# Optimization experiments

Measured on AMD Instinct MI355X. Metric: run time of the kernel, lower is better.

Reference implementation:

```python
import jax, jax.numpy as jnp
import numpy as np

N = 100000      # nodes
E = 1600000     # edges
D_IN = 128      # input feature dim
H = 128         # hidden dim
C = 2           # num classes
EPS = 1e-5


def setup_inputs() -> dict:
    key = jax.random.key(0)
    ks = jax.random.split(key, 16)
    def lin(k, fan_in, shape):
        return jax.random.uniform(k, shape, jnp.float32, -1.0, 1.0) / np.sqrt(fan_in)
    return {
        "x": jax.random.normal(ks[0], (N, D_IN), jnp.float32),
        "edge_index": jax.random.randint(ks[1], (2, E), 0, N, dtype=jnp.int32),
        # GCNConv weights (lin(x) then normalized aggregation)
        "W1": lin(ks[2], D_IN, (D_IN, H)), "b1": jnp.zeros((H,), jnp.float32),
        "W2": lin(ks[3], H, (H, H)),       "b2": jnp.zeros((H,), jnp.float32),
        "W3": lin(ks[4], H, (H, H)),       "b3": jnp.zeros((H,), jnp.float32),
        # LayerNorms after layers 0 and 1
        "ln1_g": jnp.ones((H,), jnp.float32), "ln1_b": jnp.zeros((H,), jnp.float32),
        "ln2_g": jnp.ones((H,), jnp.float32), "ln2_b": jnp.zeros((H,), jnp.float32),
        # post_mp MLP head (dropout is identity at inference)
        "mp_W1": lin(ks[5], H, (H, H)), "mp_b1": lin(ks[6], H, (H,)),
        "mp_W2": lin(ks[7], H, (H, C)), "mp_b2": lin(ks[8], H, (C,)),
    }


def _layer_norm(x, g, b):
    mu = jnp.mean(x, axis=-1, keepdims=True)
    var = jnp.mean(jnp.square(x - mu), axis=-1, keepdims=True)
    return (x - mu) * jax.lax.rsqrt(var + EPS) * g + b


def reference(x, edge_index, W1, b1, W2, b2, W3, b3,
              ln1_g, ln1_b, ln2_g, ln2_b, mp_W1, mp_b1, mp_W2, mp_b2):
    # --- GCN normalization (computed once; same graph for all layers) ---
    loops = jnp.arange(N, dtype=edge_index.dtype)
    src = jnp.concatenate([edge_index[0], loops])   # A + I, source nodes
    dst = jnp.concatenate([edge_index[1], loops])   # A + I, target nodes
    deg = jax.ops.segment_sum(jnp.ones_like(dst, dtype=x.dtype), dst, num_segments=N)
    dinv = jnp.where(deg > 0, jax.lax.rsqrt(deg), 0.0)
    norm = dinv[src] * dinv[dst]                    # [E+N]

    def gcn(h, W, b):
        h = h @ W                                   # [N, H]
        msg = h[src] * norm[:, None]                # gather + scale: [E+N, H]
        return jax.ops.segment_sum(msg, dst, num_segments=N) + b

    # layer 0
    h = gcn(x, W1, b1)
    h = jax.nn.relu(h)                              # dropout: identity (eval)
    h = _layer_norm(h, ln1_g, ln1_b)
    # layer 1
    h = gcn(h, W2, b2)
    h = jax.nn.relu(h)
    h = _layer_norm(h, ln2_g, ln2_b)
    # layer 2
    h = gcn(h, W3, b3)
    emb = h
    h = jax.nn.relu(h)

    # post_mp: Linear -> Dropout(identity at eval) -> Linear
    out = (h @ mp_W1 + mp_b1) @ mp_W2 + mp_b2
    return emb, jax.nn.log_softmax(out, axis=1)
```

## Files before the change

kernel.cpp:

```cpp
#include <hip/hip_runtime.h>
#include <math.h>

#define HDIM 128
#define EPSLN 1e-5f
#define BSH 8
#define CHUNK 8192
#define EPB 32
#define CAPB 8192

__device__ __forceinline__ unsigned short f2bf(float f) {
  unsigned int u = __float_as_uint(f);
  u = u + 0x7fffu + ((u >> 16) & 1u);
  return (unsigned short)(u >> 16);
}
__device__ __forceinline__ float bf_lo(unsigned int packed) {
  return __uint_as_float(packed << 16);
}
__device__ __forceinline__ float bf_hi(unsigned int packed) {
  return __uint_as_float(packed & 0xffff0000u);
}


__global__ __launch_bounds__(256) void histA_k(const int* __restrict__ dst,
                                               int* __restrict__ bsize, int E_) {
  __shared__ int h[512];
  int t = threadIdx.x;
  h[t] = 0; h[t + 256] = 0;
  __syncthreads();
  int base = blockIdx.x * CHUNK;
  for (int i = 0; i < EPB; i++) {
    int idx = base + i * 256 + t;
    if (idx < E_) atomicAdd(&h[dst[idx] >> BSH], 1);
  }
  __syncthreads();
  int v = h[t];       if (v) atomicAdd(&bsize[t], v);
  v = h[t + 256];     if (v) atomicAdd(&bsize[t + 256], v);
}

__global__ __launch_bounds__(256) void scanA_k(const int* __restrict__ bsize,
                                               int* __restrict__ bbase,
                                               int* __restrict__ bcur,
                                               int* __restrict__ rowptr,
                                               int NB, int n, int E_) {
  __shared__ int sm[512];
  int t = threadIdx.x;
  sm[t] = (t < NB) ? bsize[t] : 0;
  sm[t + 256] = (t + 256 < NB) ? bsize[t + 256] : 0;
  __syncthreads();
  for (int off = 1; off < 512; off <<= 1) {
    int v0 = (t >= off) ? sm[t - off] : 0;
    int v1 = (t + 256 >= off) ? sm[t + 256 - off] : 0;
    __syncthreads();
    sm[t] += v0;
    sm[t + 256] += v1;
    __syncthreads();
  }
  if (t < NB) { int ex = (t == 0) ? 0 : sm[t - 1]; bbase[t] = ex; bcur[t] = ex; }
  int u = t + 256;
  if (u < NB) { int ex = sm[u - 1]; bbase[u] = ex; bcur[u] = ex; }
  if (t == 0) { bbase[NB] = sm[NB - 1]; rowptr[n] = E_; }
}

__global__ __launch_bounds__(256) void scatA_k(const int* __restrict__ src,
                                               const int* __restrict__ dst,
                                               int* __restrict__ bcur,
                                               uint2* __restrict__ binned, int E_) {
  __shared__ int h[512];
  __shared__ int cur[512];
  int t = threadIdx.x;
  h[t] = 0; h[t + 256] = 0;
  __syncthreads();
  int base = blockIdx.x * CHUNK;
  for (int i = 0; i < EPB; i++) {
    int idx = base + i * 256 + t;
    if (idx < E_) atomicAdd(&h[dst[idx] >> BSH], 1);
  }
  __syncthreads();
  int v = h[t];       cur[t] = v ? atomicAdd(&bcur[t], v) : 0;
  v = h[t + 256];     cur[t + 256] = v ? atomicAdd(&bcur[t + 256], v) : 0;
  __syncthreads();
  for (int i = 0; i < EPB; i++) {
    int idx = base + i * 256 + t;
    if (idx < E_) {
      int d = dst[idx];
      int slot = atomicAdd(&cur[d >> BSH], 1);
      binned[slot] = make_uint2((unsigned)src[idx], (unsigned)d);
    }
  }
}

__global__ __launch_bounds__(256) void passB_k(const uint2* __restrict__ binned,
                                               const int* __restrict__ bbase,
                                               int* __restrict__ rowptr,
                                               float* __restrict__ dinv,
                                               int* __restrict__ colx, int n) {
  __shared__ int cnt[256];
  __shared__ int cur[256];
  __shared__ int stage[CAPB];
  int b = blockIdx.x;
  int t = threadIdx.x;
  int beg = bbase[b], end = bbase[b + 1];
  int sz = end - beg;
  int nb0 = b << BSH;
  cnt[t] = 0;
  __syncthreads();
  for (int i = t; i < sz; i += 256) {
    uint2 e = binned[beg + i];
    atomicAdd(&cnt[e.y & 255], 1);
  }
  __syncthreads();
  int myc = cnt[t];
  cur[t] = myc;
  __syncthreads();
  for (int off = 1; off < 256; off <<= 1) {
    int v = (t >= off) ? cur[t - off] : 0;
    __syncthreads();
    cur[t] += v;
    __syncthreads();
  }
  int excl = cur[t] - myc;
  int node = nb0 + t;
  if (node < n) {
    rowptr[node] = beg + excl;
    dinv[node] = rsqrtf((float)(myc + 1));
  }
  __syncthreads();
  cur[t] = excl;
  __syncthreads();
  if (sz <= CAPB) {
    for (int i = t; i < sz; i += 256) {
      uint2 e = binned[beg + i];
      int slot = atomicAdd(&cur[e.y & 255], 1);
      stage[slot] = (int)e.x;
    }
    __syncthreads();
    for (int i = t; i < sz; i += 256) colx[beg + i] = stage[i];
  } else {
    for (int i = t; i < sz; i += 256) {
      uint2 e = binned[beg + i];
      int slot = atomicAdd(&cur[e.y & 255], 1);
      colx[beg + slot] = (int)e.x;
    }
  }
}

__global__ __launch_bounds__(256) void gemm_k(const float* __restrict__ A,
                                              const float* __restrict__ W,
                                              const float* __restrict__ dinv,
                                              unsigned short* __restrict__ Out, int n) {
  __shared__ float hs[64 * HDIM];
  int t = threadIdx.x;
  int rowbase = blockIdx.x * 64;
  const float4* A4 = (const float4*)(A + (size_t)rowbase * HDIM);
  for (int i = 0; i < 8; i++) {
    int fi = t + i * 256;
    int row = rowbase + (fi >> 5);
    float4 v = make_float4(0.f, 0.f, 0.f, 0.f);
    if (row < n) v = A4[fi];
    ((float4*)hs)[fi] = v;
  }
  __syncthreads();

  int tc = t & 31;
  int tr = t >> 5;
  float acc[8][4];
  for (int i = 0; i < 8; i++)
    for (int j = 0; j < 4; j++) acc[i][j] = 0.f;

  const float4* W4 = (const float4*)W;
  for (int k = 0; k < HDIM; k += 4) {
    float4 w0 = W4[(k + 0) * 32 + tc];
    float4 w1 = W4[(k + 1) * 32 + tc];
    float4 w2 = W4[(k + 2) * 32 + tc];
    float4 w3 = W4[(k + 3) * 32 + tc];
    for (int i = 0; i < 8; i++) {
      float4 h4 = *((const float4*)&hs[(tr * 8 + i) * HDIM + k]);
      acc[i][0] += h4.x * w0.x + h4.y * w1.x + h4.z * w2.x + h4.w * w3.x;
      acc[i][1] += h4.x * w0.y + h4.y * w1.y + h4.z * w2.y + h4.w * w3.y;
      acc[i][2] += h4.x * w0.z + h4.y * w1.z + h4.z * w2.z + h4.w * w3.z;
      acc[i][3] += h4.x * w0.w + h4.y * w1.w + h4.z * w2.w + h4.w * w3.w;
    }
  }
  for (int i = 0; i < 8; i++) {
    int row = rowbase + tr * 8 + i;
    if (row < n) {
      float dv = dinv[row];
      ushort4 o;
      o.x = f2bf(acc[i][0] * dv);
      o.y = f2bf(acc[i][1] * dv);
      o.z = f2bf(acc[i][2] * dv);
      o.w = f2bf(acc[i][3] * dv);
      ((ushort4*)(Out + (size_t)row * HDIM))[tc] = o;
    }
  }
}

template <int MODE>
__global__ __launch_bounds__(256) void agg_k(const unsigned short* __restrict__ T,
                                             const int* __restrict__ rowptr,
                                             const int* __restrict__ colx,
                                             const float* __restrict__ dinv,
                                             const float* __restrict__ bias,
                                             const float* __restrict__ lng,
                                             const float* __restrict__ lnb,
                                             float* __restrict__ Out, int n) {
  int wid = (blockIdx.x * 256 + threadIdx.x) >> 6;
  int lane = threadIdx.x & 63;
  if (wid >= n) return;
  int i = wid;
  float di = dinv[i];
  const unsigned int* T32 = (const unsigned int*)T;
  unsigned int us = T32[(size_t)i * 64 + lane];
  float a0x = bf_lo(us), a0y = bf_hi(us);
  float a1x = 0.f, a1y = 0.f;
  int beg = rowptr[i], end = rowptr[i + 1];
  int e = beg;
  int c0 = 0, c1 = 0;
  if (e < end) c0 = colx[e];
  if (e + 1 < end) c1 = colx[e + 1];
  for (; e + 1 < end; e += 2) {
    unsigned int u0 = T32[(size_t)c0 * 64 + lane];
    unsigned int u1 = T32[(size_t)c1 * 64 + lane];
    if (e + 2 < end) c0 = colx[e + 2];
    if (e + 3 < end) c1 = colx[e + 3];
    a0x += bf_lo(u0); a0y += bf_hi(u0);
    a1x += bf_lo(u1); a1y += bf_hi(u1);
  }
  if (e < end) {
    unsigned int u0 = T32[(size_t)c0 * 64 + lane];
    a0x += bf_lo(u0); a0y += bf_hi(u0);
  }
  float2 bb = ((const float2*)bias)[lane];
  float2 acc;
  acc.x = (a0x + a1x) * di + bb.x;
  acc.y = (a0y + a1y) * di + bb.y;
  if (MODE == 0) {
    acc.x = fmaxf(acc.x, 0.f);
    acc.y = fmaxf(acc.y, 0.f);
    float s1 = acc.x + acc.y;
    float s2 = acc.x * acc.x + acc.y * acc.y;
    for (int off = 1; off < 64; off <<= 1) {
      s1 += __shfl_xor(s1, off);
      s2 += __shfl_xor(s2, off);
    }
    float mu = s1 * (1.f / 128.f);
    float var = s2 * (1.f / 128.f) - mu * mu;
    float r = rsqrtf(var + EPSLN);
    float2 gg = ((const float2*)lng)[lane];
    float2 b2 = ((const float2*)lnb)[lane];
    acc.x = (acc.x - mu) * r * gg.x + b2.x;
    acc.y = (acc.y - mu) * r * gg.y + b2.y;
  }
  ((float2*)(Out + (size_t)i * HDIM))[lane] = acc;
}

__global__ __launch_bounds__(256) void head_k(const float* __restrict__ emb,
                                              const float* __restrict__ W1_,
                                              const float* __restrict__ b1_,
                                              const float* __restrict__ W2_,
                                              const float* __restrict__ b2_,
                                              float* __restrict__ outp, int n) {
  __shared__ float hs[64 * HDIM];
  int t = threadIdx.x;
  int rowbase = blockIdx.x * 64;
  const float4* A4 = (const float4*)(emb + (size_t)rowbase * HDIM);
  for (int i = 0; i < 8; i++) {
    int fi = t + i * 256;
    int row = rowbase + (fi >> 5);
    float4 v = make_float4(0.f, 0.f, 0.f, 0.f);
    if (row < n) v = A4[fi];
    v.x = fmaxf(v.x, 0.f);
    v.y = fmaxf(v.y, 0.f);
    v.z = fmaxf(v.z, 0.f);
    v.w = fmaxf(v.w, 0.f);
    ((float4*)hs)[fi] = v;
  }
  __syncthreads();

  int tc = t & 31;
  int tr = t >> 5;
  float acc[8][4];
  float4 binit = ((const float4*)b1_)[tc];
  for (int i = 0; i < 8; i++) {
    acc[i][0] = binit.x; acc[i][1] = binit.y; acc[i][2] = binit.z; acc[i][3] = binit.w;
  }

  const float4* W4 = (const float4*)W1_;
  for (int k = 0; k < HDIM; k += 4) {
    float4 w0 = W4[(k + 0) * 32 + tc];
    float4 w1 = W4[(k + 1) * 32 + tc];
    float4 w2 = W4[(k + 2) * 32 + tc];
    float4 w3 = W4[(k + 3) * 32 + tc];
    for (int i = 0; i < 8; i++) {
      float4 h4 = *((const float4*)&hs[(tr * 8 + i) * HDIM + k]);
      acc[i][0] += h4.x * w0.x + h4.y * w1.x + h4.z * w2.x + h4.w * w3.x;
      acc[i][1] += h4.x * w0.y + h4.y * w1.y + h4.z * w2.y + h4.w * w3.y;
      acc[i][2] += h4.x * w0.z + h4.y * w1.z + h4.z * w2.z + h4.w * w3.z;
      acc[i][3] += h4.x * w0.w + h4.y * w1.w + h4.z * w2.w + h4.w * w3.w;
    }
  }

  float2 w2c[4];
  for (int j = 0; j < 4; j++) w2c[j] = ((const float2*)W2_)[4 * tc + j];
  float o0[8], o1[8];
  for (int i = 0; i < 8; i++) {
    o0[i] = acc[i][0] * w2c[0].x + acc[i][1] * w2c[1].x + acc[i][2] * w2c[2].x + acc[i][3] * w2c[3].x;
    o1[i] = acc[i][0] * w2c[0].y + acc[i][1] * w2c[1].y + acc[i][2] * w2c[2].y + acc[i][3] * w2c[3].y;
  }
  for (int off = 1; off < 32; off <<= 1) {
    for (int i = 0; i < 8; i++) {
      o0[i] += __shfl_xor(o0[i], off);
      o1[i] += __shfl_xor(o1[i], off);
    }
  }
  if (tc == 0) {
    float B0 = b2_[0], B1 = b2_[1];
    for (int i = 0; i < 8; i++) {
      int row = rowbase + tr * 8 + i;
      if (row < n) {
        float a = o0[i] + B0, b = o1[i] + B1;
        float m = fmaxf(a, b);
        float lse = m + logf(expf(a - m) + expf(b - m));
        outp[(size_t)row * 2 + 0] = a - lse;
        outp[(size_t)row * 2 + 1] = b - lse;
      }
    }
  }
}


extern "C" void kernel_launch(void* const* d_in, const int* in_sizes, int n_in,
                              void* d_out, int out_size, void* d_ws, size_t ws_size,
                              hipStream_t stream) {
  const float* x = (const float*)d_in[0];
  const int* ei = (const int*)d_in[1];
  const float* W1 = (const float*)d_in[2];
  const float* b1 = (const float*)d_in[3];
  const float* W2 = (const float*)d_in[4];
  const float* b2 = (const float*)d_in[5];
  const float* W3 = (const float*)d_in[6];
  const float* b3 = (const float*)d_in[7];
  const float* ln1g = (const float*)d_in[8];
  const float* ln1b = (const float*)d_in[9];
  const float* ln2g = (const float*)d_in[10];
  const float* ln2b = (const float*)d_in[11];
  const float* mpW1 = (const float*)d_in[12];
  const float* mpb1 = (const float*)d_in[13];
  const float* mpW2 = (const float*)d_in[14];
  const float* mpb2 = (const float*)d_in[15];

  const int N = in_sizes[0] / HDIM;
  const int E = in_sizes[1] / 2;
  const int* srcp = ei;
  const int* dstp = ei + E;
  const int NB = (N + 255) >> BSH;

  char* p = (char*)d_ws;
  auto carve = [&](size_t bytes) {
    void* r = (void*)p;
    p += (bytes + 255) & ~(size_t)255;
    return r;
  };
  int* bsize = (int*)carve(512 * 4);
  int* bbase = (int*)carve(513 * 4);
  int* bcur = (int*)carve(512 * 4);
  int* rowptr = (int*)carve((size_t)(N + 1) * 4);
  float* dinv = (float*)carve((size_t)N * 4);
  int* colx = (int*)carve((size_t)E * 4);
  uint2* binned = (uint2*)carve((size_t)E * 8);
  unsigned short* bufT = (unsigned short*)carve((size_t)N * HDIM * 2);
  float* bufAct = (float*)carve((size_t)N * HDIM * 4);

  float* emb = (float*)d_out;
  float* logits = (float*)d_out + (size_t)N * HDIM;

  const int chunkG = (E + CHUNK - 1) / CHUNK;

  hipMemsetAsync(bsize, 0, 512 * 4, stream);
  histA_k<<<chunkG, 256, 0, stream>>>(dstp, bsize, E);
  scanA_k<<<1, 256, 0, stream>>>(bsize, bbase, bcur, rowptr, NB, N, E);
  scatA_k<<<chunkG, 256, 0, stream>>>(srcp, dstp, bcur, binned, E);
  passB_k<<<NB, 256, 0, stream>>>(binned, bbase, rowptr, dinv, colx, N);

  const int gemmG = (N + 63) / 64;
  const int aggG = (N * 64 + 255) / 256;

  gemm_k<<<gemmG, 256, 0, stream>>>(x, W1, dinv, bufT, N);
  agg_k<0><<<aggG, 256, 0, stream>>>(bufT, rowptr, colx, dinv, b1, ln1g, ln1b, bufAct, N);
  gemm_k<<<gemmG, 256, 0, stream>>>(bufAct, W2, dinv, bufT, N);
  agg_k<0><<<aggG, 256, 0, stream>>>(bufT, rowptr, colx, dinv, b2, ln2g, ln2b, bufAct, N);
  gemm_k<<<gemmG, 256, 0, stream>>>(bufAct, W3, dinv, bufT, N);
  agg_k<1><<<aggG, 256, 0, stream>>>(bufT, rowptr, colx, dinv, b3, nullptr, nullptr, emb, N);
  head_k<<<gemmG, 256, 0, stream>>>(emb, mpW1, mpb1, mpW2, mpb2, logits, N);
}
```

Baseline: 689.0 us.

## Rewrite feature-transform GEMM with bf16 MFMA and 128-row tiles

The per-layer N×128×128 GEMM is moved from FP32 scalar FMAs to bf16 MFMA 16x16x32 instructions. Activations and weights are converted to bf16 into padded LDS tiles (transposed for W), and each block now covers 128 rows. Each wave handles 32 rows across all 128 output columns. Inputs are rounded to bf16 before the multiply, which lowers precision, and the output is written as scattered 2-byte stores. Each block also re-converts the whole weight matrix.

```diff
diff --git a/kernel.cpp b/kernel.cpp
--- a/kernel.cpp
+++ b/kernel.cpp
@@ -7,6 +7,10 @@
 #define CHUNK 8192
 #define EPB 32
 #define CAPB 8192
+#define LDA 136
+
+typedef __attribute__((ext_vector_type(8))) short bf16x8;
+typedef __attribute__((ext_vector_type(4))) float f32x4;
 
 __device__ __forceinline__ unsigned short f2bf(float f) {
   unsigned int u = __float_as_uint(f);
@@ -148,49 +152,81 @@
                                               const float* __restrict__ W,
                                               const float* __restrict__ dinv,
                                               unsigned short* __restrict__ Out, int n) {
-  __shared__ float hs[64 * HDIM];
-  int t = threadIdx.x;
-  int rowbase = blockIdx.x * 64;
-  const float4* A4 = (const float4*)(A + (size_t)rowbase * HDIM);
-  for (int i = 0; i < 8; i++) {
-    int fi = t + i * 256;
-    int row = rowbase + (fi >> 5);
+  __shared__ short As[128 * LDA];
+  __shared__ short Ws[128 * LDA];
+  int t = threadIdx.x;
+  int rowbase = blockIdx.x * 128;
+
+  #pragma unroll
+  for (int i = 0; i < 64; i++) {
+    int idx = t + i * 256;
+    int k = idx >> 7, c = idx & 127;
+    Ws[c * LDA + k] = (short)f2bf(W[idx]);
+  }
+  const float4* A4 = (const float4*)A;
+  #pragma unroll
+  for (int i = 0; i < 16; i++) {
+    int idx = t + i * 256;
+    int r = idx >> 5, c4 = (idx & 31) << 2;
+    int grow = rowbase + r;
     float4 v = make_float4(0.f, 0.f, 0.f, 0.f);
-    if (row < n) v = A4[fi];
-    ((float4*)hs)[fi] = v;
-  }
-  __syncthreads();
-
-  int tc = t & 31;
-  int tr = t >> 5;
-  float acc[8][4];
-  for (int i = 0; i < 8; i++)
-    for (int j = 0; j < 4; j++) acc[i][j] = 0.f;
-
-  const float4* W4 = (const float4*)W;
-  for (int k = 0; k < HDIM; k += 4) {
-    float4 w0 = W4[(k + 0) * 32 + tc];
-    float4 w1 = W4[(k + 1) * 32 + tc];
-    float4 w2 = W4[(k + 2) * 32 + tc];
-    float4 w3 = W4[(k + 3) * 32 + tc];
-    for (int i = 0; i < 8; i++) {
-      float4 h4 = *((const float4*)&hs[(tr * 8 + i) * HDIM + k]);
-      acc[i][0] += h4.x * w0.x + h4.y * w1.x + h4.z * w2.x + h4.w * w3.x;
-      acc[i][1] += h4.x * w0.y + h4.y * w1.y + h4.z * w2.y + h4.w * w3.y;
-      acc[i][2] += h4.x * w0.z + h4.y * w1.z + h4.z * w2.z + h4.w * w3.z;
-      acc[i][3] += h4.x * w0.w + h4.y * w1.w + h4.z * w2.w + h4.w * w3.w;
-    }
-  }
-  for (int i = 0; i < 8; i++) {
-    int row = rowbase + tr * 8 + i;
-    if (row < n) {
-      float dv = dinv[row];
-      ushort4 o;
-      o.x = f2bf(acc[i][0] * dv);
-      o.y = f2bf(acc[i][1] * dv);
-      o.z = f2bf(acc[i][2] * dv);
-      o.w = f2bf(acc[i][3] * dv);
-      ((ushort4*)(Out + (size_t)row * HDIM))[tc] = o;
+    if (grow < n) v = A4[(size_t)grow * 32 + (idx & 31)];
+    short4 s;
+    s.x = (short)f2bf(v.x); s.y = (short)f2bf(v.y);
+    s.z = (short)f2bf(v.z); s.w = (short)f2bf(v.w);
+    *(short4*)&As[r * LDA + c4] = s;
+  }
+  __syncthreads();
+
+  int wv = t >> 6;
+  int lane = t & 63;
+  int lrow = lane & 15;
+  int lk = (lane >> 4) << 3;
+  int wr0 = wv * 32;
+
+  const short* base0 = &As[(wr0 + lrow) * LDA + lk];
+  const short* base1 = &As[(wr0 + 16 + lrow) * LDA + lk];
+  bf16x8 a00 = *(const bf16x8*)(base0 + 0);
+  bf16x8 a01 = *(const bf16x8*)(base0 + 32);
+  bf16x8 a02 = *(const bf16x8*)(base0 + 64);
+  bf16x8 a03 = *(const bf16x8*)(base0 + 96);
+  bf16x8 a10 = *(const bf16x8*)(base1 + 0);
+  bf16x8 a11 = *(const bf16x8*)(base1 + 32);
+  bf16x8 a12 = *(const bf16x8*)(base1 + 64);
+  bf16x8 a13 = *(const bf16x8*)(base1 + 96);
+
+  int r0 = rowbase + wr0 + ((lane >> 4) << 2);
+  float dv0[4], dv1[4];
+  #pragma unroll
+  for (int r = 0; r < 4; r++) {
+    int g0 = r0 + r, g1 = r0 + 16 + r;
+    dv0[r] = (g0 < n) ? dinv[g0] : 0.f;
+    dv1[r] = (g1 < n) ? dinv[g1] : 0.f;
+  }
+
+  #pragma unroll
+  for (int nt = 0; nt < 8; nt++) {
+    const short* bb = &Ws[(nt * 16 + lrow) * LDA + lk];
+    f32x4 acc0 = {0.f, 0.f, 0.f, 0.f};
+    f32x4 acc1 = {0.f, 0.f, 0.f, 0.f};
+    bf16x8 b0 = *(const bf16x8*)(bb + 0);
+    acc0 = __builtin_amdgcn_mfma_f32_16x16x32_bf16(a00, b0, acc0, 0, 0, 0);
+    acc1 = __builtin_amdgcn_mfma_f32_16x16x32_bf16(a10, b0, acc1, 0, 0, 0);
+    bf16x8 b1 = *(const bf16x8*)(bb + 32);
+    acc0 = __builtin_amdgcn_mfma_f32_16x16x32_bf16(a01, b1, acc0, 0, 0, 0);
+    acc1 = __builtin_amdgcn_mfma_f32_16x16x32_bf16(a11, b1, acc1, 0, 0, 0);
+    bf16x8 b2 = *(const bf16x8*)(bb + 64);
+    acc0 = __builtin_amdgcn_mfma_f32_16x16x32_bf16(a02, b2, acc0, 0, 0, 0);
+    acc1 = __builtin_amdgcn_mfma_f32_16x16x32_bf16(a12, b2, acc1, 0, 0, 0);
+    bf16x8 b3 = *(const bf16x8*)(bb + 96);
+    acc0 = __builtin_amdgcn_mfma_f32_16x16x32_bf16(a03, b3, acc0, 0, 0, 0);
+    acc1 = __builtin_amdgcn_mfma_f32_16x16x32_bf16(a13, b3, acc1, 0, 0, 0);
+    #pragma unroll
+    for (int r = 0; r < 4; r++) {
+      int g0 = r0 + r;
+      if (g0 < n) Out[(size_t)g0 * HDIM + nt * 16 + lrow] = f2bf(acc0[r] * dv0[r]);
+      int g1 = r0 + 16 + r;
+      if (g1 < n) Out[(size_t)g1 * HDIM + nt * 16 + lrow] = f2bf(acc1[r] * dv1[r]);
     }
   }
 }
@@ -382,7 +418,8 @@
   scatA_k<<<chunkG, 256, 0, stream>>>(srcp, dstp, bcur, binned, E);
   passB_k<<<NB, 256, 0, stream>>>(binned, bbase, rowptr, dinv, colx, N);
 
-  const int gemmG = (N + 63) / 64;
+  const int gemmG = (N + 127) / 128;
+  const int headG = (N + 63) / 64;
   const int aggG = (N * 64 + 255) / 256;
 
   gemm_k<<<gemmG, 256, 0, stream>>>(x, W1, dinv, bufT, N);
@@ -391,5 +428,5 @@
   agg_k<0><<<aggG, 256, 0, stream>>>(bufT, rowptr, colx, dinv, b2, ln2g, ln2b, bufAct, N);
   gemm_k<<<gemmG, 256, 0, stream>>>(bufAct, W3, dinv, bufT, N);
   agg_k<1><<<aggG, 256, 0, stream>>>(bufT, rowptr, colx, dinv, b3, nullptr, nullptr, emb, N);
-  head_k<<<gemmG, 256, 0, stream>>>(emb, mpW1, mpb1, mpW2, mpb2, logits, N);
-}
+  head_k<<<headG, 256, 0, stream>>>(emb, mpW1, mpb1, mpW2, mpb2, logits, N);
+}
```

New measurement: 621.3 us. -9.8%, faster.
